# Performance work log

Hardware: AMD Instinct MI355X
Metric: run time of the kernel (lower is better)

Reference implementation:

```python
import jax, jax.numpy as jnp
import numpy as np

VOC, OUT, HID, CUR = 50257, 512, 64, 16
B, S = 32, 4096
EPS = 1e-5


def _ln(x, g, b):
    m = jnp.mean(x, axis=-1, keepdims=True)
    v = jnp.mean((x - m) ** 2, axis=-1, keepdims=True)
    return (x - m) * jax.lax.rsqrt(v + EPS) * g + b


def setup_inputs() -> dict:
    key = jax.random.key(0)
    ks = jax.random.split(key, 12)
    sd = 0.02
    return {
        "x": jax.random.randint(ks[0], (B, S), 0, VOC, dtype=jnp.int64),
        "emb": jax.random.normal(ks[1], (VOC, CUR), jnp.float32) * sd,
        "Wq": jax.random.normal(ks[2], (CUR, CUR), jnp.float32) * sd,
        "bq": jnp.zeros((CUR,), jnp.float32),
        "Wk": jax.random.normal(ks[3], (CUR, CUR), jnp.float32) * sd,
        "bk": jnp.zeros((CUR,), jnp.float32),
        "Wv": jax.random.normal(ks[4], (CUR, CUR), jnp.float32) * sd,
        "bv": jnp.zeros((CUR,), jnp.float32),
        "g_lim": jnp.ones((CUR,), jnp.float32),
        "b_lim": jnp.zeros((CUR,), jnp.float32),
        "Ws": jax.random.normal(ks[5], (HID + CUR, HID), jnp.float32) * sd,
        "bs": jnp.zeros((HID,), jnp.float32),
        "g_doubt": jnp.ones((HID,), jnp.float32),
        "b_doubt": jnp.zeros((HID,), jnp.float32),
        "Wd": jax.random.normal(ks[6], (HID + CUR, OUT), jnp.float32) * sd,
        "bd": jnp.zeros((OUT,), jnp.float32),
        "g_check": jnp.ones((OUT,), jnp.float32),
        "b_check": jnp.zeros((OUT,), jnp.float32),
    }


def reference(x, emb, Wq, bq, Wk, bk, Wv, bv, g_lim, b_lim, Ws, bs,
              g_doubt, b_doubt, Wd, bd, g_check, b_check):
    Bsz, Slen = x.shape
    n_chunks = Slen // CUR
    # [n_chunks, B, CUR] token ids per chunk
    xc = x.reshape(Bsz, n_chunks, CUR).transpose(1, 0, 2)
    sus0 = jnp.zeros((Bsz, CUR, HID), emb.dtype)
    scale = 1.0 / np.sqrt(CUR)

    def step(sus, ids):
        read = emb[ids]                                  # [B, CUR, CUR]
        q = read @ Wq + bq
        k = read @ Wk + bk
        v = read @ Wv + bv
        scores = jnp.einsum('bqd,bkd->bqk', q, k) * scale
        watch = jnp.einsum('bqk,bkd->bqd', jax.nn.softmax(scores, axis=-1), v)
        watch = _ln(watch, g_lim, b_lim)                 # dropout = identity (eval)
        combined = jnp.concatenate([watch, sus], axis=-1)  # [B, CUR, HID+CUR]
        sus_new = _ln(jax.nn.gelu(combined @ Ws + bs, approximate=False),
                      g_doubt, b_doubt)
        out = _ln(combined @ Wd + bd, g_check, b_check)  # [B, CUR, OUT]
        return sus_new, out

    _, outs = jax.lax.scan(step, sus0, xc)               # [n_chunks, B, CUR, OUT]
    return outs.transpose(1, 0, 2, 3).reshape(Bsz, Slen, OUT)
```

## Files before the change

kernel.cpp:

```cpp
#include <hip/hip_runtime.h>
#include <math.h>

#define VOCN 50257
#define OUTD 512
#define HIDD 64
#define CURD 16
#define BB   32
#define SS   4096
#define NCH  256
#define KDIM 80
#define LNEPS 1e-5f

__global__ __launch_bounds__(256) void attn_kernel(
    const int* __restrict__ x, const float* __restrict__ emb,
    const float* __restrict__ Wq, const float* __restrict__ bq,
    const float* __restrict__ Wk, const float* __restrict__ bk,
    const float* __restrict__ Wv, const float* __restrict__ bv,
    const float* __restrict__ g_lim, const float* __restrict__ b_lim,
    float* __restrict__ combined)
{
    const int wid  = threadIdx.x >> 6;
    const int lane = threadIdx.x & 63;
    const int tile = blockIdx.x * 4 + wid;
    const int t = tile >> 5, b = tile & 31;
    const int i  = lane >> 2;
    const int jg = lane & 3;
    const int j0 = jg * 4;

    __shared__ __align__(16) float ldsT[4][4][16][20];
    float (*R)[20] = ldsT[wid][0];
    float (*Q)[20] = ldsT[wid][1];
    float (*K)[20] = ldsT[wid][2];
    float (*V)[20] = ldsT[wid][3];

    int myid = 0;
    if (lane < 16) myid = x[b * SS + t * CURD + lane];
    const int id_i = __shfl(myid, i, 64);

    float4 r4 = *(const float4*)(emb + (size_t)id_i * CURD + j0);
    *(float4*)&R[i][j0] = r4;

    float rrow[16];
    {
        float4 t0 = *(const float4*)&R[i][0];
        float4 t1 = *(const float4*)&R[i][4];
        float4 t2 = *(const float4*)&R[i][8];
        float4 t3 = *(const float4*)&R[i][12];
        rrow[0]=t0.x; rrow[1]=t0.y; rrow[2]=t0.z;  rrow[3]=t0.w;
        rrow[4]=t1.x; rrow[5]=t1.y; rrow[6]=t1.z;  rrow[7]=t1.w;
        rrow[8]=t2.x; rrow[9]=t2.y; rrow[10]=t2.z; rrow[11]=t2.w;
        rrow[12]=t3.x; rrow[13]=t3.y; rrow[14]=t3.z; rrow[15]=t3.w;
    }

    float4 q4 = *(const float4*)(bq + j0);
    float4 k4 = *(const float4*)(bk + j0);
    float4 v4 = *(const float4*)(bv + j0);
    #pragma unroll
    for (int k = 0; k < 16; ++k) {
        float rv = rrow[k];
        float4 wq4 = *(const float4*)(Wq + k * CURD + j0);
        float4 wk4 = *(const float4*)(Wk + k * CURD + j0);
        float4 wv4 = *(const float4*)(Wv + k * CURD + j0);
        q4.x = fmaf(rv, wq4.x, q4.x); q4.y = fmaf(rv, wq4.y, q4.y);
        q4.z = fmaf(rv, wq4.z, q4.z); q4.w = fmaf(rv, wq4.w, q4.w);
        k4.x = fmaf(rv, wk4.x, k4.x); k4.y = fmaf(rv, wk4.y, k4.y);
        k4.z = fmaf(rv, wk4.z, k4.z); k4.w = fmaf(rv, wk4.w, k4.w);
        v4.x = fmaf(rv, wv4.x, v4.x); v4.y = fmaf(rv, wv4.y, v4.y);
        v4.z = fmaf(rv, wv4.z, v4.z); v4.w = fmaf(rv, wv4.w, v4.w);
    }
    *(float4*)&Q[i][j0] = q4;
    *(float4*)&K[i][j0] = k4;
    *(float4*)&V[i][j0] = v4;

    float qrow[16];
    {
        float4 t0 = *(const float4*)&Q[i][0];
        float4 t1 = *(const float4*)&Q[i][4];
        float4 t2 = *(const float4*)&Q[i][8];
        float4 t3 = *(const float4*)&Q[i][12];
        qrow[0]=t0.x; qrow[1]=t0.y; qrow[2]=t0.z;  qrow[3]=t0.w;
        qrow[4]=t1.x; qrow[5]=t1.y; qrow[6]=t1.z;  qrow[7]=t1.w;
        qrow[8]=t2.x; qrow[9]=t2.y; qrow[10]=t2.z; qrow[11]=t2.w;
        qrow[12]=t3.x; qrow[13]=t3.y; qrow[14]=t3.z; qrow[15]=t3.w;
    }
    float sc[4];
    #pragma unroll
    for (int jj = 0; jj < 4; ++jj) {
        const int row = j0 + jj;
        float4 c0 = *(const float4*)&K[row][0];
        float4 c1 = *(const float4*)&K[row][4];
        float4 c2 = *(const float4*)&K[row][8];
        float4 c3 = *(const float4*)&K[row][12];
        float d0 = qrow[0]*c0.x + qrow[1]*c0.y + qrow[2]*c0.z + qrow[3]*c0.w;
        float d1 = qrow[4]*c1.x + qrow[5]*c1.y + qrow[6]*c1.z + qrow[7]*c1.w;
        float d2 = qrow[8]*c2.x + qrow[9]*c2.y + qrow[10]*c2.z + qrow[11]*c2.w;
        float d3 = qrow[12]*c3.x + qrow[13]*c3.y + qrow[14]*c3.z + qrow[15]*c3.w;
        sc[jj] = ((d0 + d1) + (d2 + d3)) * 0.25f;
    }

    float mx = fmaxf(fmaxf(sc[0], sc[1]), fmaxf(sc[2], sc[3]));
    mx = fmaxf(mx, __shfl_xor(mx, 1));
    mx = fmaxf(mx, __shfl_xor(mx, 2));
    float e0 = expf(sc[0]-mx), e1 = expf(sc[1]-mx),
          e2 = expf(sc[2]-mx), e3 = expf(sc[3]-mx);
    float es = (e0 + e1) + (e2 + e3);
    es += __shfl_xor(es, 1);
    es += __shfl_xor(es, 2);
    float rs = 1.f / es;
    float4 p4 = make_float4(e0*rs, e1*rs, e2*rs, e3*rs);
    *(float4*)&R[i][j0] = p4;

    float prow[16];
    {
        float4 t0 = *(const float4*)&R[i][0];
        float4 t1 = *(const float4*)&R[i][4];
        float4 t2 = *(const float4*)&R[i][8];
        float4 t3 = *(const float4*)&R[i][12];
        prow[0]=t0.x; prow[1]=t0.y; prow[2]=t0.z;  prow[3]=t0.w;
        prow[4]=t1.x; prow[5]=t1.y; prow[6]=t1.z;  prow[7]=t1.w;
        prow[8]=t2.x; prow[9]=t2.y; prow[10]=t2.z; prow[11]=t2.w;
        prow[12]=t3.x; prow[13]=t3.y; prow[14]=t3.z; prow[15]=t3.w;
    }
    float4 w4 = make_float4(0.f, 0.f, 0.f, 0.f);
    #pragma unroll
    for (int k = 0; k < 16; ++k) {
        float4 vk = *(const float4*)&V[k][j0];
        float pv = prow[k];
        w4.x = fmaf(pv, vk.x, w4.x); w4.y = fmaf(pv, vk.y, w4.y);
        w4.z = fmaf(pv, vk.z, w4.z); w4.w = fmaf(pv, vk.w, w4.w);
    }

    float s1 = (w4.x + w4.y) + (w4.z + w4.w);
    float s2 = (w4.x*w4.x + w4.y*w4.y) + (w4.z*w4.z + w4.w*w4.w);
    s1 += __shfl_xor(s1, 1); s1 += __shfl_xor(s1, 2);
    s2 += __shfl_xor(s2, 1); s2 += __shfl_xor(s2, 2);
    float m   = s1 * (1.f / 16.f);
    float var = s2 * (1.f / 16.f) - m * m;
    float inv = rsqrtf(var + LNEPS);
    float4 gl = *(const float4*)(g_lim + j0);
    float4 bl = *(const float4*)(b_lim + j0);
    float4 o;
    o.x = (w4.x - m) * inv * gl.x + bl.x;
    o.y = (w4.y - m) * inv * gl.y + bl.y;
    o.z = (w4.z - m) * inv * gl.z + bl.z;
    o.w = (w4.w - m) * inv * gl.w + bl.w;
    *(float4*)(combined + ((size_t)tile * CURD + i) * KDIM + j0) = o;
}

__global__ __launch_bounds__(64) void rec_kernel(
    const float* __restrict__ Ws, const float* __restrict__ bs,
    const float* __restrict__ g_doubt, const float* __restrict__ b_doubt,
    float* __restrict__ combined)
{
    const int chain = blockIdx.x;
    const int b = chain >> 4;
    const int r = chain & 15;
    const int c = threadIdx.x;

    __shared__ __align__(16) float s_G[64];
    __shared__ __align__(16) float s_watch[16];

    float Wsw[16];
    #pragma unroll
    for (int j = 0; j < 16; ++j) Wsw[j] = Ws[j * HIDD + c];

    float Wsp[64];
    float u = 0.f, w0 = 0.f;
    #pragma unroll
    for (int j = 0; j < 64; ++j) {
        float w   = Ws[(16 + j) * HIDD + c];
        float gdj = g_doubt[j];
        float bdj = b_doubt[j];
        Wsp[j] = gdj * w;
        u += Wsp[j];
        w0 = fmaf(bdj, w, w0);
    }
    const float bsc  = bs[c];
    const float gd_c = g_doubt[c];
    const float bd_c = b_doubt[c];

    float P = 0.f, mp = 0.f, ip = 0.f, w0f = 0.f;
    float sv_store = 0.f;
    float wv = (c < 16) ? combined[((size_t)b * CURD + r) * KDIM + c] : 0.f;

    size_t rowoff = ((size_t)b * CURD + r) * KDIM;
    const size_t stride = (size_t)BB * CURD * KDIM;

    for (int t = 0; t < NCH; ++t) {
        combined[rowoff + 16 + c] = sv_store;
        if (c < 16) s_watch[c] = wv;
        float wv_next = 0.f;
        if (t + 1 < NCH && c < 16) wv_next = combined[rowoff + stride + c];

        float h0 = fmaf(ip, P - mp * u, bsc + w0f);
        float h1 = 0.f, h2 = 0.f, h3 = 0.f;
        {
            const float4* wp4 = (const float4*)s_watch;
            float4 a0 = wp4[0], a1 = wp4[1], a2 = wp4[2], a3 = wp4[3];
            h0 = fmaf(a0.x, Wsw[0],  h0); h1 = fmaf(a0.y, Wsw[1],  h1);
            h2 = fmaf(a0.z, Wsw[2],  h2); h3 = fmaf(a0.w, Wsw[3],  h3);
            h0 = fmaf(a1.x, Wsw[4],  h0); h1 = fmaf(a1.y, Wsw[5],  h1);
            h2 = fmaf(a1.z, Wsw[6],  h2); h3 = fmaf(a1.w, Wsw[7],  h3);
            h0 = fmaf(a2.x, Wsw[8],  h0); h1 = fmaf(a2.y, Wsw[9],  h1);
            h2 = fmaf(a2.z, Wsw[10], h2); h3 = fmaf(a2.w, Wsw[11], h3);
            h0 = fmaf(a3.x, Wsw[12], h0); h1 = fmaf(a3.y, Wsw[13], h1);
            h2 = fmaf(a3.z, Wsw[14], h2); h3 = fmaf(a3.w, Wsw[15], h3);
        }
        float h = (h0 + h1) + (h2 + h3);

        float G = 0.5f * h * (1.f + erff(h * 0.70710678118654752f));

        s_G[c] = G;
        const float4* gp = (const float4*)s_G;
        float4 xr[16];
        #pragma unroll
        for (int j4 = 0; j4 < 16; ++j4) xr[j4] = gp[j4];

        float s1 = G, s2 = G * G;
        #pragma unroll
        for (int off = 32; off; off >>= 1) {
            s1 += __shfl_xor(s1, off, 64);
            s2 += __shfl_xor(s2, off, 64);
        }
        float m   = s1 * (1.f / 64.f);
        float var = s2 * (1.f / 64.f) - m * m;
        float inv = rsqrtf(var + LNEPS);

        float p0=0.f,p1=0.f,p2=0.f,p3=0.f,p4=0.f,p5=0.f,p6=0.f,p7=0.f;
        #pragma unroll
        for (int j4 = 0; j4 < 16; j4 += 2) {
            float4 x0 = xr[j4], x1 = xr[j4 + 1];
            p0 = fmaf(x0.x, Wsp[4*j4+0], p0);
            p1 = fmaf(x0.y, Wsp[4*j4+1], p1);
            p2 = fmaf(x0.z, Wsp[4*j4+2], p2);
            p3 = fmaf(x0.w, Wsp[4*j4+3], p3);
            p4 = fmaf(x1.x, Wsp[4*j4+4], p4);
            p5 = fmaf(x1.y, Wsp[4*j4+5], p5);
            p6 = fmaf(x1.z, Wsp[4*j4+6], p6);
            p7 = fmaf(x1.w, Wsp[4*j4+7], p7);
        }
        P = ((p0 + p1) + (p2 + p3)) + ((p4 + p5) + (p6 + p7));

        sv_store = fmaf((G - m) * inv, gd_c, bd_c);
        mp = m; ip = inv; w0f = w0;
        wv = wv_next;
        rowoff += stride;
    }
}

#define R3 32
__global__ __launch_bounds__(256) void out_kernel(
    const float* __restrict__ combined, const float* __restrict__ Wd,
    const float* __restrict__ bd, const float* __restrict__ g_check,
    const float* __restrict__ b_check, float* __restrict__ out)
{
    __shared__ float At[R3][84];

    const int tid  = threadIdx.x;
    const int lane = tid & 63;
    const int rg   = tid >> 6;
    const size_t rowbase = (size_t)blockIdx.x * R3;

    const float4* src4 = (const float4*)(combined + rowbase * KDIM);
    #pragma unroll
    for (int u = 0; u < 3; ++u) {
        int idx = tid + 256 * u;
        if (idx < R3 * 20) {
            float4 vv = src4[idx];
            int rr = idx / 20, kk4 = idx % 20;
            *(float4*)&At[rr][kk4 * 4] = vv;
        }
    }
    __syncthreads();

    const int c0 = lane * 8;
    float acc[8][8];
    #pragma unroll
    for (int rr = 0; rr < 8; ++rr)
        #pragma unroll
        for (int cc = 0; cc < 8; ++cc) acc[rr][cc] = 0.f;

    for (int k4 = 0; k4 < 20; ++k4) {
        const float* wp = Wd + (size_t)(k4 * 4) * OUTD + c0;
        float4 wa[4], wb[4];
        #pragma unroll
        for (int kk = 0; kk < 4; ++kk) {
            wa[kk] = *(const float4*)(wp + kk * OUTD);
            wb[kk] = *(const float4*)(wp + kk * OUTD + 4);
        }
        #pragma unroll
        for (int rr = 0; rr < 8; ++rr) {
            float4 a = *(const float4*)&At[rg * 8 + rr][k4 * 4];
            float av[4] = {a.x, a.y, a.z, a.w};
            #pragma unroll
            for (int kk = 0; kk < 4; ++kk) {
                acc[rr][0] = fmaf(av[kk], wa[kk].x, acc[rr][0]);
                acc[rr][1] = fmaf(av[kk], wa[kk].y, acc[rr][1]);
                acc[rr][2] = fmaf(av[kk], wa[kk].z, acc[rr][2]);
                acc[rr][3] = fmaf(av[kk], wa[kk].w, acc[rr][3]);
                acc[rr][4] = fmaf(av[kk], wb[kk].x, acc[rr][4]);
                acc[rr][5] = fmaf(av[kk], wb[kk].y, acc[rr][5]);
                acc[rr][6] = fmaf(av[kk], wb[kk].z, acc[rr][6]);
                acc[rr][7] = fmaf(av[kk], wb[kk].w, acc[rr][7]);
            }
        }
    }

    float4 bda = *(const float4*)(bd + c0);
    float4 bdb = *(const float4*)(bd + c0 + 4);
    float4 ga  = *(const float4*)(g_check + c0);
    float4 gb  = *(const float4*)(g_check + c0 + 4);
    float4 ba  = *(const float4*)(b_check + c0);
    float4 bb  = *(const float4*)(b_check + c0 + 4);
    const float bav[8] = {bda.x, bda.y, bda.z, bda.w, bdb.x, bdb.y, bdb.z, bdb.w};
    const float gav[8] = {ga.x, ga.y, ga.z, ga.w, gb.x, gb.y, gb.z, gb.w};
    const float cav[8] = {ba.x, ba.y, ba.z, ba.w, bb.x, bb.y, bb.z, bb.w};

    #pragma unroll
    for (int rr = 0; rr < 8; ++rr) {
        float s1 = 0.f, s2 = 0.f;
        #pragma unroll
        for (int cc = 0; cc < 8; ++cc) {
            float vv = acc[rr][cc] + bav[cc];
            acc[rr][cc] = vv;
            s1 += vv;
            s2 += vv * vv;
        }
        #pragma unroll
        for (int off = 32; off; off >>= 1) {
            s1 += __shfl_xor(s1, off, 64);
            s2 += __shfl_xor(s2, off, 64);
        }
        float m   = s1 * (1.f / 512.f);
        float var = s2 * (1.f / 512.f) - m * m;
        float inv = rsqrtf(var + LNEPS);

        size_t R = rowbase + (size_t)rg * 8 + rr;
        int ii  = (int)(R & 15);
        int bb2 = (int)((R >> 4) & 31);
        int tt  = (int)(R >> 9);
        size_t orow = (size_t)bb2 * SS + (size_t)tt * CURD + ii;

        float4 o0, o1;
        o0.x = (acc[rr][0] - m) * inv * gav[0] + cav[0];
        o0.y = (acc[rr][1] - m) * inv * gav[1] + cav[1];
        o0.z = (acc[rr][2] - m) * inv * gav[2] + cav[2];
        o0.w = (acc[rr][3] - m) * inv * gav[3] + cav[3];
        o1.x = (acc[rr][4] - m) * inv * gav[4] + cav[4];
        o1.y = (acc[rr][5] - m) * inv * gav[5] + cav[5];
        o1.z = (acc[rr][6] - m) * inv * gav[6] + cav[6];
        o1.w = (acc[rr][7] - m) * inv * gav[7] + cav[7];
        *(float4*)(out + orow * OUTD + c0)     = o0;
        *(float4*)(out + orow * OUTD + c0 + 4) = o1;
    }
}

extern "C" void kernel_launch(void* const* d_in, const int* in_sizes, int n_in,
                              void* d_out, int out_size, void* d_ws, size_t ws_size,
                              hipStream_t stream)
{
    const int*   x       = (const int*)  d_in[0];
    const float* emb     = (const float*)d_in[1];
    const float* Wq      = (const float*)d_in[2];
    const float* bq      = (const float*)d_in[3];
    const float* Wk      = (const float*)d_in[4];
    const float* bk      = (const float*)d_in[5];
    const float* Wv      = (const float*)d_in[6];
    const float* bv      = (const float*)d_in[7];
    const float* g_lim   = (const float*)d_in[8];
    const float* b_lim   = (const float*)d_in[9];
    const float* Ws      = (const float*)d_in[10];
    const float* bs      = (const float*)d_in[11];
    const float* g_doubt = (const float*)d_in[12];
    const float* b_doubt = (const float*)d_in[13];
    const float* Wd      = (const float*)d_in[14];
    const float* bd      = (const float*)d_in[15];
    const float* g_check = (const float*)d_in[16];
    const float* b_check = (const float*)d_in[17];

    float* out      = (float*)d_out;
    float* combined = (float*)d_ws;

    attn_kernel<<<dim3(NCH * BB / 4), dim3(256), 0, stream>>>(
        x, emb, Wq, bq, Wk, bk, Wv, bv, g_lim, b_lim, combined);

    rec_kernel<<<dim3(BB * CURD), dim3(64), 0, stream>>>(
        Ws, bs, g_doubt, b_doubt, combined);

    out_kernel<<<dim3((NCH * BB * CURD) / R3), dim3(256), 0, stream>>>(
        combined, Wd, bd, g_check, b_check, out);
}
```

Baseline: 579.1 us.

## Use split-bf16 MFMA for output projection and DPP reductions in recurrence

Replaces the FP32 FMA output projection with bf16 MFMA 16x16x32 instructions. Each operand is split into hi/lo bf16 parts so accuracy stays close to fp32 (three MFMAs per product). A small pack kernel pre-splits Wd into a blocked layout. The recurrence kernel now prefetches the watch rows two steps ahead straight into registers instead of going through LDS, and uses DPP/readlane reductions for the LayerNorm sums. The cost is an extra launch, extra conversion work and a larger workspace region.

```diff
diff --git a/kernel.cpp b/kernel.cpp
--- a/kernel.cpp
+++ b/kernel.cpp
@@ -10,6 +10,55 @@
 #define NCH  256
 #define KDIM 80
 #define LNEPS 1e-5f
+
+#define DPP_ADD(x, ctrl) \
+    ((x) + __int_as_float(__builtin_amdgcn_update_dpp( \
+        0, __float_as_int(x), (ctrl), 0xf, 0xf, true)))
+
+__device__ __forceinline__ float row16_sum(float x) {
+    x = DPP_ADD(x, 0xB1);
+    x = DPP_ADD(x, 0x4E);
+    x = DPP_ADD(x, 0x141);
+    x = DPP_ADD(x, 0x140);
+    return x;
+}
+
+__device__ __forceinline__ float wave64_sum(float x) {
+    float r = row16_sum(x);
+    float a = __int_as_float(__builtin_amdgcn_readlane(__float_as_int(r), 0));
+    float b = __int_as_float(__builtin_amdgcn_readlane(__float_as_int(r), 16));
+    float c = __int_as_float(__builtin_amdgcn_readlane(__float_as_int(r), 32));
+    float d = __int_as_float(__builtin_amdgcn_readlane(__float_as_int(r), 48));
+    return (a + b) + (c + d);
+}
+
+__device__ __forceinline__ unsigned short f2bf(float x) {
+    unsigned u = __float_as_uint(x);
+    u += 0x7fffu + ((u >> 16) & 1u);
+    return (unsigned short)(u >> 16);
+}
+__device__ __forceinline__ float bf2f(unsigned short h) {
+    return __uint_as_float(((unsigned)h) << 16);
+}
+
+typedef __attribute__((ext_vector_type(8))) short bf16x8;
+typedef __attribute__((ext_vector_type(4))) float f32x4;
+
+__global__ __launch_bounds__(256) void wd_pack_kernel(
+    const float* __restrict__ Wd,
+    unsigned short* __restrict__ hi, unsigned short* __restrict__ lo)
+{
+    int idx = blockIdx.x * 256 + threadIdx.x;
+    if (idx >= 96 * 512) return;
+    int k = idx / 512, c = idx % 512;
+    float v = (k < KDIM) ? Wd[(size_t)k * OUTD + c] : 0.f;
+    unsigned short h = f2bf(v);
+    unsigned short l = f2bf(v - bf2f(h));
+    int s = k >> 5, kk = k & 31, g = kk >> 3, e = kk & 7;
+    size_t o = (((size_t)(s * 512 + c)) * 4 + g) * 8 + e;
+    hi[o] = h;
+    lo[o] = l;
+}
 
 __global__ __launch_bounds__(256) void attn_kernel(
     const int* __restrict__ x, const float* __restrict__ emb,
@@ -158,7 +207,6 @@
     const int c = threadIdx.x;
 
     __shared__ __align__(16) float s_G[64];
-    __shared__ __align__(16) float s_watch[16];
 
     float Wsw[16];
     #pragma unroll
@@ -179,33 +227,42 @@
     const float gd_c = g_doubt[c];
     const float bd_c = b_doubt[c];
 
+    size_t rowoff = ((size_t)b * CURD + r) * KDIM;
+    const size_t stride = (size_t)BB * CURD * KDIM;
+
+    float4 wc0, wc1, wc2, wc3;
+    float4 wn0, wn1, wn2, wn3;
+    {
+        const float4* p0 = (const float4*)(combined + rowoff);
+        wc0 = p0[0]; wc1 = p0[1]; wc2 = p0[2]; wc3 = p0[3];
+        const float4* p1 = (const float4*)(combined + rowoff + stride);
+        wn0 = p1[0]; wn1 = p1[1]; wn2 = p1[2]; wn3 = p1[3];
+    }
+
     float P = 0.f, mp = 0.f, ip = 0.f, w0f = 0.f;
     float sv_store = 0.f;
-    float wv = (c < 16) ? combined[((size_t)b * CURD + r) * KDIM + c] : 0.f;
-
-    size_t rowoff = ((size_t)b * CURD + r) * KDIM;
-    const size_t stride = (size_t)BB * CURD * KDIM;
 
     for (int t = 0; t < NCH; ++t) {
         combined[rowoff + 16 + c] = sv_store;
-        if (c < 16) s_watch[c] = wv;
-        float wv_next = 0.f;
-        if (t + 1 < NCH && c < 16) wv_next = combined[rowoff + stride + c];
+
+        float4 wp0, wp1, wp2, wp3;
+        if (t + 2 < NCH) {
+            const float4* p2 = (const float4*)(combined + rowoff + 2 * stride);
+            wp0 = p2[0]; wp1 = p2[1]; wp2 = p2[2]; wp3 = p2[3];
+        } else {
+            wp0 = wp1 = wp2 = wp3 = make_float4(0.f, 0.f, 0.f, 0.f);
+        }
 
         float h0 = fmaf(ip, P - mp * u, bsc + w0f);
         float h1 = 0.f, h2 = 0.f, h3 = 0.f;
-        {
-            const float4* wp4 = (const float4*)s_watch;
-            float4 a0 = wp4[0], a1 = wp4[1], a2 = wp4[2], a3 = wp4[3];
-            h0 = fmaf(a0.x, Wsw[0],  h0); h1 = fmaf(a0.y, Wsw[1],  h1);
-            h2 = fmaf(a0.z, Wsw[2],  h2); h3 = fmaf(a0.w, Wsw[3],  h3);
-            h0 = fmaf(a1.x, Wsw[4],  h0); h1 = fmaf(a1.y, Wsw[5],  h1);
-            h2 = fmaf(a1.z, Wsw[6],  h2); h3 = fmaf(a1.w, Wsw[7],  h3);
-            h0 = fmaf(a2.x, Wsw[8],  h0); h1 = fmaf(a2.y, Wsw[9],  h1);
-            h2 = fmaf(a2.z, Wsw[10], h2); h3 = fmaf(a2.w, Wsw[11], h3);
-            h0 = fmaf(a3.x, Wsw[12], h0); h1 = fmaf(a3.y, Wsw[13], h1);
-            h2 = fmaf(a3.z, Wsw[14], h2); h3 = fmaf(a3.w, Wsw[15], h3);
-        }
+        h0 = fmaf(wc0.x, Wsw[0],  h0); h1 = fmaf(wc0.y, Wsw[1],  h1);
+        h2 = fmaf(wc0.z, Wsw[2],  h2); h3 = fmaf(wc0.w, Wsw[3],  h3);
+        h0 = fmaf(wc1.x, Wsw[4],  h0); h1 = fmaf(wc1.y, Wsw[5],  h1);
+        h2 = fmaf(wc1.z, Wsw[6],  h2); h3 = fmaf(wc1.w, Wsw[7],  h3);
+        h0 = fmaf(wc2.x, Wsw[8],  h0); h1 = fmaf(wc2.y, Wsw[9],  h1);
+        h2 = fmaf(wc2.z, Wsw[10], h2); h3 = fmaf(wc2.w, Wsw[11], h3);
+        h0 = fmaf(wc3.x, Wsw[12], h0); h1 = fmaf(wc3.y, Wsw[13], h1);
+        h2 = fmaf(wc3.z, Wsw[14], h2); h3 = fmaf(wc3.w, Wsw[15], h3);
         float h = (h0 + h1) + (h2 + h3);
 
         float G = 0.5f * h * (1.f + erff(h * 0.70710678118654752f));
@@ -216,12 +273,8 @@
         #pragma unroll
         for (int j4 = 0; j4 < 16; ++j4) xr[j4] = gp[j4];
 
-        float s1 = G, s2 = G * G;
-        #pragma unroll
-        for (int off = 32; off; off >>= 1) {
-            s1 += __shfl_xor(s1, off, 64);
-            s2 += __shfl_xor(s2, off, 64);
-        }
+        float s1 = wave64_sum(G);
+        float s2 = wave64_sum(G * G);
         float m   = s1 * (1.f / 64.f);
         float var = s2 * (1.f / 64.f) - m * m;
         float inv = rsqrtf(var + LNEPS);
@@ -243,115 +296,154 @@
 
         sv_store = fmaf((G - m) * inv, gd_c, bd_c);
         mp = m; ip = inv; w0f = w0;
-        wv = wv_next;
+        wc0 = wn0; wc1 = wn1; wc2 = wn2; wc3 = wn3;
+        wn0 = wp0; wn1 = wp1; wn2 = wp2; wn3 = wp3;
         rowoff += stride;
     }
 }
 
-#define R3 32
-__global__ __launch_bounds__(256) void out_kernel(
-    const float* __restrict__ combined, const float* __restrict__ Wd,
+#define M_BLK 32
+__global__ __launch_bounds__(256) void out_mfma_kernel(
+    const float* __restrict__ combined,
+    const unsigned short* __restrict__ Bhi,
+    const unsigned short* __restrict__ Blo,
     const float* __restrict__ bd, const float* __restrict__ g_check,
     const float* __restrict__ b_check, float* __restrict__ out)
 {
-    __shared__ float At[R3][84];
-
-    const int tid  = threadIdx.x;
-    const int lane = tid & 63;
-    const int rg   = tid >> 6;
-    const size_t rowbase = (size_t)blockIdx.x * R3;
-
-    const float4* src4 = (const float4*)(combined + rowbase * KDIM);
-    #pragma unroll
-    for (int u = 0; u < 3; ++u) {
-        int idx = tid + 256 * u;
-        if (idx < R3 * 20) {
-            float4 vv = src4[idx];
-            int rr = idx / 20, kk4 = idx % 20;
-            *(float4*)&At[rr][kk4 * 4] = vv;
-        }
-    }
+    __shared__ __align__(16) unsigned short Ahi[M_BLK][104];
+    __shared__ __align__(16) unsigned short Alo[M_BLK][104];
+    __shared__ float red[4][M_BLK][2];
+
+    const int tid = threadIdx.x;
+    const size_t rowbase = (size_t)blockIdx.x * M_BLK;
+
+    {
+        const float4* src4 = (const float4*)(combined + rowbase * KDIM);
+        #pragma unroll
+        for (int u2 = 0; u2 < 3; ++u2) {
+            int idx = tid + 256 * u2;
+            if (idx < M_BLK * 20) {
+                float4 v = src4[idx];
+                int rr = idx / 20, k4 = idx % 20;
+                float vs[4] = {v.x, v.y, v.z, v.w};
+                #pragma unroll
+                for (int e = 0; e < 4; ++e) {
+                    unsigned short h = f2bf(vs[e]);
+                    Ahi[rr][k4 * 4 + e] = h;
+                    Alo[rr][k4 * 4 + e] = f2bf(vs[e] - bf2f(h));
+                }
+            }
+        }
+        #pragma unroll
+        for (int u2 = 0; u2 < 2; ++u2) {
+            int idx = tid + 256 * u2;
+            int rr = idx >> 4, kk = 80 + (idx & 15);
+            Ahi[rr][kk] = 0;
+            Alo[rr][kk] = 0;
+        }
+    }
+
+    const int lane  = tid & 63;
+    const int wid   = tid >> 6;
+    const int arowb = lane & 15;
+    const int kg    = lane >> 4;
+
+    int cols[8]; float bdv[8], gcv[8], bcv[8];
+    #pragma unroll
+    for (int n = 0; n < 8; ++n) {
+        cols[n] = wid * 128 + n * 16 + arowb;
+        bdv[n] = bd[cols[n]];
+        gcv[n] = g_check[cols[n]];
+        bcv[n] = b_check[cols[n]];
+    }
+
     __syncthreads();
 
-    const int c0 = lane * 8;
-    float acc[8][8];
-    #pragma unroll
-    for (int rr = 0; rr < 8; ++rr)
-        #pragma unroll
-        for (int cc = 0; cc < 8; ++cc) acc[rr][cc] = 0.f;
-
-    for (int k4 = 0; k4 < 20; ++k4) {
-        const float* wp = Wd + (size_t)(k4 * 4) * OUTD + c0;
-        float4 wa[4], wb[4];
-        #pragma unroll
-        for (int kk = 0; kk < 4; ++kk) {
-            wa[kk] = *(const float4*)(wp + kk * OUTD);
-            wb[kk] = *(const float4*)(wp + kk * OUTD + 4);
-        }
-        #pragma unroll
-        for (int rr = 0; rr < 8; ++rr) {
-            float4 a = *(const float4*)&At[rg * 8 + rr][k4 * 4];
-            float av[4] = {a.x, a.y, a.z, a.w};
+    bf16x8 a_hi[2][3], a_lo[2][3];
+    #pragma unroll
+    for (int ms = 0; ms < 2; ++ms)
+        #pragma unroll
+        for (int s = 0; s < 3; ++s) {
+            a_hi[ms][s] = *(const bf16x8*)&Ahi[ms * 16 + arowb][s * 32 + kg * 8];
+            a_lo[ms][s] = *(const bf16x8*)&Alo[ms * 16 + arowb][s * 32 + kg * 8];
+        }
+
+    f32x4 acc[2][8];
+    #pragma unroll
+    for (int ms = 0; ms < 2; ++ms)
+        #pragma unroll
+        for (int n = 0; n < 8; ++n) acc[ms][n] = (f32x4){0.f, 0.f, 0.f, 0.f};
+
+    #pragma unroll
+    for (int n = 0; n < 8; ++n) {
+        #pragma unroll
+        for (int s = 0; s < 3; ++s) {
+            size_t off = (((size_t)(s * 512 + cols[n])) * 4 + kg) * 8;
+            bf16x8 bh = *(const bf16x8*)(Bhi + off);
+            bf16x8 bl = *(const bf16x8*)(Blo + off);
+            acc[0][n] = __builtin_amdgcn_mfma_f32_16x16x32_bf16(a_hi[0][s], bh, acc[0][n], 0, 0, 0);
+            acc[1][n] = __builtin_amdgcn_mfma_f32_16x16x32_bf16(a_hi[1][s], bh, acc[1][n], 0, 0, 0);
+            acc[0][n] = __builtin_amdgcn_mfma_f32_16x16x32_bf16(a_lo[0][s], bh, acc[0][n], 0, 0, 0);
+            acc[1][n] = __builtin_amdgcn_mfma_f32_16x16x32_bf16(a_lo[1][s], bh, acc[1][n], 0, 0, 0);
+            acc[0][n] = __builtin_amdgcn_mfma_f32_16x16x32_bf16(a_hi[0][s], bl, acc[0][n], 0, 0, 0);
+            acc[1][n] = __builtin_amdgcn_mfma_f32_16x16x32_bf16(a_hi[1][s], bl, acc[1][n], 0, 0, 0);
+        }
+    }
+
+    #pragma unroll
+    for (int ms = 0; ms < 2; ++ms) {
+        float s1[4] = {0.f, 0.f, 0.f, 0.f};
+        float s2[4] = {0.f, 0.f, 0.f, 0.f};
+        #pragma unroll
+        for (int n = 0; n < 8; ++n) {
             #pragma unroll
-            for (int kk = 0; kk < 4; ++kk) {
-                acc[rr][0] = fmaf(av[kk], wa[kk].x, acc[rr][0]);
-                acc[rr][1] = fmaf(av[kk], wa[kk].y, acc[rr][1]);
-                acc[rr][2] = fmaf(av[kk], wa[kk].z, acc[rr][2]);
-                acc[rr][3] = fmaf(av[kk], wa[kk].w, acc[rr][3]);
-                acc[rr][4] = fmaf(av[kk], wb[kk].x, acc[rr][4]);
-                acc[rr][5] = fmaf(av[kk], wb[kk].y, acc[rr][5]);
-                acc[rr][6] = fmaf(av[kk], wb[kk].z, acc[rr][6]);
-                acc[rr][7] = fmaf(av[kk], wb[kk].w, acc[rr][7]);
+            for (int j = 0; j < 4; ++j) {
+                float v = acc[ms][n][j] + bdv[n];
+                acc[ms][n][j] = v;
+                s1[j] += v;
+                s2[j] = fmaf(v, v, s2[j]);
             }
         }
-    }
-
-    float4 bda = *(const float4*)(bd + c0);
-    float4 bdb = *(const float4*)(bd + c0 + 4);
-    float4 ga  = *(const float4*)(g_check + c0);
-    float4 gb  = *(const float4*)(g_check + c0 + 4);
-    float4 ba  = *(const float4*)(b_check + c0);
-    float4 bb  = *(const float4*)(b_check + c0 + 4);
-    const float bav[8] = {bda.x, bda.y, bda.z, bda.w, bdb.x, bdb.y, bdb.z, bdb.w};
-    const float gav[8] = {ga.x, ga.y, ga.z, ga.w, gb.x, gb.y, gb.z, gb.w};
-    const float cav[8] = {ba.x, ba.y, ba.z, ba.w, bb.x, bb.y, bb.z, bb.w};
-
-    #pragma unroll
-    for (int rr = 0; rr < 8; ++rr) {
-        float s1 = 0.f, s2 = 0.f;
-        #pragma unroll
-        for (int cc = 0; cc < 8; ++cc) {
-            float vv = acc[rr][cc] + bav[cc];
-            acc[rr][cc] = vv;
-            s1 += vv;
-            s2 += vv * vv;
-        }
-        #pragma unroll
-        for (int off = 32; off; off >>= 1) {
-            s1 += __shfl_xor(s1, off, 64);
-            s2 += __shfl_xor(s2, off, 64);
-        }
-        float m   = s1 * (1.f / 512.f);
-        float var = s2 * (1.f / 512.f) - m * m;
-        float inv = rsqrtf(var + LNEPS);
-
-        size_t R = rowbase + (size_t)rg * 8 + rr;
-        int ii  = (int)(R & 15);
-        int bb2 = (int)((R >> 4) & 31);
-        int tt  = (int)(R >> 9);
-        size_t orow = (size_t)bb2 * SS + (size_t)tt * CURD + ii;
-
-        float4 o0, o1;
-        o0.x = (acc[rr][0] - m) * inv * gav[0] + cav[0];
-        o0.y = (acc[rr][1] - m) * inv * gav[1] + cav[1];
-        o0.z = (acc[rr][2] - m) * inv * gav[2] + cav[2];
-        o0.w = (acc[rr][3] - m) * inv * gav[3] + cav[3];
-        o1.x = (acc[rr][4] - m) * inv * gav[4] + cav[4];
-        o1.y = (acc[rr][5] - m) * inv * gav[5] + cav[5];
-        o1.z = (acc[rr][6] - m) * inv * gav[6] + cav[6];
-        o1.w = (acc[rr][7] - m) * inv * gav[7] + cav[7];
-        *(float4*)(out + orow * OUTD + c0)     = o0;
-        *(float4*)(out + orow * OUTD + c0 + 4) = o1;
+        #pragma unroll
+        for (int j = 0; j < 4; ++j) {
+            s1[j] = row16_sum(s1[j]);
+            s2[j] = row16_sum(s2[j]);
+        }
+        if (arowb == 0) {
+            #pragma unroll
+            for (int j = 0; j < 4; ++j) {
+                red[wid][ms * 16 + kg * 4 + j][0] = s1[j];
+                red[wid][ms * 16 + kg * 4 + j][1] = s2[j];
+            }
+        }
+    }
+    __syncthreads();
+
+    #pragma unroll
+    for (int ms = 0; ms < 2; ++ms) {
+        #pragma unroll
+        for (int j = 0; j < 4; ++j) {
+            const int rowl = ms * 16 + kg * 4 + j;
+            float t1 = (red[0][rowl][0] + red[1][rowl][0])
+                     + (red[2][rowl][0] + red[3][rowl][0]);
+            float t2 = (red[0][rowl][1] + red[1][rowl][1])
+                     + (red[2][rowl][1] + red[3][rowl][1]);
+            float mm  = t1 * (1.f / 512.f);
+            float var = t2 * (1.f / 512.f) - mm * mm;
+            float iv  = rsqrtf(var + LNEPS);
+
+            size_t R = rowbase + (size_t)rowl;
+            int ii  = (int)(R & 15);
+            int bb2 = (int)((R >> 4) & 31);
+            int tt  = (int)(R >> 9);
+            size_t orow = ((size_t)bb2 * SS + (size_t)tt * CURD + ii) * OUTD;
+
+            #pragma unroll
+            for (int n = 0; n < 8; ++n) {
+                out[orow + cols[n]] =
+                    (acc[ms][n][j] - mm) * iv * gcv[n] + bcv[n];
+            }
+        }
     }
 }
 
@@ -380,6 +472,10 @@
 
     float* out      = (float*)d_out;
     float* combined = (float*)d_ws;
+    unsigned short* whi = (unsigned short*)((char*)d_ws + 41943040);
+    unsigned short* wlo = whi + 96 * 512;
+
+    wd_pack_kernel<<<dim3(192), dim3(256), 0, stream>>>(Wd, whi, wlo);
 
     attn_kernel<<<dim3(NCH * BB / 4), dim3(256), 0, stream>>>(
         x, emb, Wq, bq, Wk, bk, Wv, bv, g_lim, b_lim, combined);
@@ -387,6 +483,6 @@
     rec_kernel<<<dim3(BB * CURD), dim3(64), 0, stream>>>(
         Ws, bs, g_doubt, b_doubt, combined);
 
-    out_kernel<<<dim3((NCH * BB * CURD) / R3), dim3(256), 0, stream>>>(
-        combined, Wd, bd, g_check, b_check, out);
-}
+    out_mfma_kernel<<<dim3((NCH * BB * CURD) / M_BLK), dim3(256), 0, stream>>>(
+        combined, whi, wlo, bd, g_check, b_check, out);
+}
```

New measurement: 503.5 us. -13.1%, faster.
